# Kernel optimization log

Hardware: AMD Instinct MI355X
Metric: run time of the kernel (lower is better)

Reference implementation:

```python
import jax, jax.numpy as jnp
import numpy as np

B, S, H = 2, 2048, 2048
NH, KVH, HD = 32, 8, 64
G = NH // KVH
BASE = 10000.0
SCALE = 1.0 / np.sqrt(HD).astype(np.float32)


def _rope_cache(seq_len, dim, base):
    inv_freq = 1.0 / (base ** (jnp.arange(0, dim, 2, dtype=jnp.float32) / dim))
    t = jnp.arange(seq_len, dtype=jnp.float32)
    freqs = jnp.outer(t, inv_freq)            # [S, HD/2]
    emb = jnp.concatenate([freqs, freqs], -1)  # [S, HD]
    return jnp.cos(emb), jnp.sin(emb)


def _rotate_half(x):
    x1, x2 = jnp.split(x, 2, axis=-1)
    return jnp.concatenate([-x2, x1], axis=-1)


def setup_inputs() -> dict:
    key = jax.random.key(0)
    ks = jax.random.split(key, 5)
    hidden_states = jax.random.normal(ks[0], (B, S, H), jnp.float32)
    # additive causal mask, broadcast over heads
    causal = jnp.tril(jnp.ones((S, S), dtype=bool))
    attention_mask = jnp.where(causal, 0.0, -1e9).astype(jnp.float32)[None, None]
    attention_mask = jnp.broadcast_to(attention_mask, (B, 1, S, S))
    position_ids = jnp.broadcast_to(jnp.arange(S, dtype=jnp.int32), (B, S))
    w = 0.02
    Wq = jax.random.normal(ks[1], (H, NH * HD), jnp.float32) * w
    Wk = jax.random.normal(ks[2], (H, KVH * HD), jnp.float32) * w
    Wv = jax.random.normal(ks[3], (H, KVH * HD), jnp.float32) * w
    Wo = jax.random.normal(ks[4], (NH * HD, H), jnp.float32) * w
    return {"hidden_states": hidden_states, "attention_mask": attention_mask,
            "position_ids": position_ids, "Wq": Wq, "Wk": Wk, "Wv": Wv, "Wo": Wo}


def reference(hidden_states, attention_mask, position_ids, Wq, Wk, Wv, Wo):
    b, s, _ = hidden_states.shape
    q = (hidden_states @ Wq).reshape(b, s, NH, HD).transpose(0, 2, 1, 3)   # [B,NH,S,HD]
    k = (hidden_states @ Wk).reshape(b, s, KVH, HD).transpose(0, 2, 1, 3)  # [B,KVH,S,HD]
    v = (hidden_states @ Wv).reshape(b, s, KVH, HD).transpose(0, 2, 1, 3)
    cos_c, sin_c = _rope_cache(s, HD, BASE)
    cos = cos_c[position_ids][:, None]  # [B,1,S,HD]
    sin = sin_c[position_ids][:, None]
    q = q * cos + _rotate_half(q) * sin
    k = k * cos + _rotate_half(k) * sin
    # GQA: grouped einsum == repeat_kv + matmul (same math, no KV duplication)
    qg = q.reshape(b, KVH, G, s, HD)
    scores = jnp.einsum('bkgsd,bktd->bkgst', qg, k) * SCALE  # [B,KVH,G,S,S]
    scores = scores + attention_mask[:, :, None]             # mask [B,1,1,S,S]
    probs = jax.nn.softmax(scores.astype(jnp.float32), axis=-1).astype(q.dtype)
    ctx = jnp.einsum('bkgst,bktd->bkgsd', probs, v)
    ctx = ctx.reshape(b, NH, s, HD).transpose(0, 2, 1, 3).reshape(b, s, NH * HD)
    return ctx @ Wo
```

## Files before the change

kernel.cpp:

```cpp
#include <hip/hip_runtime.h>
#include <hip/hip_bf16.h>

#define DB   2
#define DS   2048
#define DH   2048
#define DNH  32
#define DKVH 8
#define DHD  64
#define DM   4096
#define DNQKV 3072

typedef __attribute__((ext_vector_type(8))) short bf16x8;
typedef __attribute__((ext_vector_type(4))) float f32x4;
typedef __attribute__((ext_vector_type(8))) unsigned short us8;
typedef __attribute__((ext_vector_type(4))) unsigned short us4;
typedef __attribute__((ext_vector_type(2))) unsigned int u32x2;

__device__ __forceinline__ float b2f(unsigned short u) {
  unsigned int x = ((unsigned int)u) << 16;
  return __builtin_bit_cast(float, x);
}
__device__ __forceinline__ unsigned short f2b(float f) {
  unsigned int u = __builtin_bit_cast(unsigned int, f);
  return (unsigned short)((u + 0x8000u) >> 16);
}
__device__ __forceinline__ unsigned int cvt_pk_bf16(float lo, float hi) {
  unsigned int r;
  asm("v_cvt_pk_bf16_f32 %0, %1, %2" : "=v"(r) : "v"(lo), "v"(hi));
  return r;
}
__device__ __forceinline__ void async_copy16(void* lds, const void* g) {
  __builtin_amdgcn_global_load_lds((const __attribute__((address_space(1))) void*)g,
                                   (__attribute__((address_space(3))) void*)lds,
                                   16, 0, 0);
}

#define BARRIER() do { asm volatile("" ::: "memory"); __builtin_amdgcn_s_barrier(); asm volatile("" ::: "memory"); } while (0)
#define LGKM0()   asm volatile("s_waitcnt lgkmcnt(0)" ::: "memory")
#define WAITVM(n) asm volatile("s_waitcnt vmcnt(" #n ")" ::: "memory")
#define MFMA16(d, a, bb) (d) = __builtin_amdgcn_mfma_f32_16x16x32_bf16((a), (bb), (d), 0, 0, 0)

__device__ __forceinline__ int detect_inline(const unsigned short* __restrict__ w) {
  int t = threadIdx.x & 63;
  int trips = 0;
#pragma unroll
  for (int i = 0; i < 4; i++) {
    unsigned short u = w[t * 4 + i];
    int e = (u >> 7) & 0xFF;
    if (e >= 161 || (e <= 93 && e != 0)) trips++;
  }
#pragma unroll
  for (int off = 32; off > 0; off >>= 1) trips += __shfl_down(trips, off);
  return __shfl(trips, 0) >= 8;
}

__global__ __launch_bounds__(256)
void prep(const void* __restrict__ hs, const void* __restrict__ wq,
          const void* __restrict__ wk, const void* __restrict__ wv,
          const void* __restrict__ wo,
          unsigned short* __restrict__ xb, unsigned short* __restrict__ wtqkv,
          unsigned short* __restrict__ wto) {
  __shared__ float tile[32][33];
  int mode = detect_inline((const unsigned short*)wq);
  int bid = blockIdx.x;
  if (bid < 4096) {
    int i = (bid * 256 + threadIdx.x) * 8;
    if (mode) {
      const float* f = (const float*)hs;
      us8 o;
#pragma unroll
      for (int j = 0; j < 8; j++) o[j] = f2b(f[i + j]);
      *(us8*)&xb[i] = o;
    } else {
      *(us8*)&xb[i] = *(const us8*)((const unsigned short*)hs + i);
    }
    return;
  }
  const void* win; unsigned short* out; int C, bx, by;
  if (bid < 8192)       { int l = bid - 4096;  win = wq; out = wtqkv;                         C = 2048; bx = l & 63; by = l >> 6; }
  else if (bid < 9216)  { int l = bid - 8192;  win = wk; out = wtqkv + (size_t)2048 * 2048;   C = 512;  bx = l & 15; by = l >> 4; }
  else if (bid < 10240) { int l = bid - 9216;  win = wv; out = wtqkv + (size_t)2560 * 2048;   C = 512;  bx = l & 15; by = l >> 4; }
  else                  { int l = bid - 10240; win = wo; out = wto;                           C = 2048; bx = l & 63; by = l >> 6; }
  int c0 = bx * 32, r0 = by * 32;
  int tx = threadIdx.x & 31, ty = threadIdx.x >> 5;
  if (mode) {
    const float* f = (const float*)win;
    for (int i = ty; i < 32; i += 8) tile[i][tx] = f[(size_t)(r0 + i) * C + c0 + tx];
  } else {
    const unsigned short* bsrc = (const unsigned short*)win;
    for (int i = ty; i < 32; i += 8) tile[i][tx] = b2f(bsrc[(size_t)(r0 + i) * C + c0 + tx]);
  }
  __syncthreads();
  for (int i = ty; i < 32; i += 8) out[(size_t)(c0 + i) * 2048 + r0 + tx] = f2b(tile[tx][i]);
}

#define QSC 0.18033688011112042f

__global__ __launch_bounds__(512, 2)
void gemm_qkv(const unsigned short* __restrict__ A, const unsigned short* __restrict__ Bt,
              const int* __restrict__ pos_ids,
              unsigned short* __restrict__ qws, unsigned short* __restrict__ kws,
              unsigned short* __restrict__ vt) {
  __shared__ __align__(16) unsigned short sm[65536];
  int tid = threadIdx.x, lane = tid & 63, wave = tid >> 6;
  int wm = wave >> 2, wn = wave & 3;
  int quad = lane >> 4, l15 = lane & 15;

  int bid = blockIdx.x;
  int wg = (bid & 7) * 24 + (bid >> 3);
  int ty = wg / 12, tx = wg - ty * 12;
  size_t tm0 = (size_t)ty * 256, tn0 = (size_t)tx * 256;

  const unsigned short* Ab = A + tm0 * 2048;
  const unsigned short* Bb = Bt + tn0 * 2048;

  auto UA = [&](int bu, int kh) { return sm + (bu * 2 + kh) * 8192; };
  auto UB = [&](int bu, int kh) { return sm + 32768 + (bu * 2 + kh) * 8192; };

  int c0 = tid, c1 = tid + 512;
  int r0s = c0 >> 2, r1s = c1 >> 2;
  int cc0 = (c0 & 3) ^ ((r0s >> 1) & 3);
  int cc1 = (c1 & 3) ^ ((r1s >> 1) & 3);
  size_t ga0 = (size_t)r0s * 2048 + cc0 * 8;
  size_t ga1 = (size_t)r1s * 2048 + cc1 * 8;

  auto stA = [&](int t, int kh, int bu) {
    const unsigned short* s = Ab + (size_t)t * 64 + kh * 32;
    async_copy16(UA(bu, kh) + c0 * 8, s + ga0);
    async_copy16(UA(bu, kh) + c1 * 8, s + ga1);
  };
  auto stB = [&](int t, int kh, int bu) {
    const unsigned short* s = Bb + (size_t)t * 64 + kh * 32;
    async_copy16(UB(bu, kh) + c0 * 8, s + ga0);
    async_copy16(UB(bu, kh) + c1 * 8, s + ga1);
  };

  int rdoff = l15 * 32 + ((quad << 3) ^ (((l15 >> 1) & 3) << 3));

  f32x4 zero4 = {0.f, 0.f, 0.f, 0.f};
  f32x4 acc[8][4];
#pragma unroll
  for (int mi = 0; mi < 8; mi++)
#pragma unroll
    for (int ni = 0; ni < 4; ni++) acc[mi][ni] = zero4;

  stA(0, 0, 0); stB(0, 0, 0); stA(0, 1, 0); stB(0, 1, 0); stA(1, 0, 1); stB(1, 0, 1);
  WAITVM(8); BARRIER();

#pragma unroll 2
  for (int t = 0; t < 32; ++t) {
    int bu = t & 1, bn = bu ^ 1;
    int t1 = (t + 1 < 32) ? t + 1 : 31;
    int t2 = (t + 2 < 32) ? t + 2 : 31;
    bf16x8 af[8];
    const unsigned short* pA0 = UA(bu, 0) + wm * 4096 + rdoff;
    const unsigned short* pB0 = UB(bu, 0) + wn * 2048 + rdoff;
    const unsigned short* pA1 = UA(bu, 1) + wm * 4096 + rdoff;
    const unsigned short* pB1 = UB(bu, 1) + wn * 2048 + rdoff;

#pragma unroll
    for (int mi = 0; mi < 8; mi++) af[mi] = *(const bf16x8*)(pA0 + mi * 512);
    bf16x8 b0 = *(const bf16x8*)pB0;
    bf16x8 b1 = *(const bf16x8*)(pB0 + 512);
    stA(t1, 1, bn);
    BARRIER(); LGKM0();
    __builtin_amdgcn_s_setprio(1);
#pragma unroll
    for (int mi = 0; mi < 8; mi++) { MFMA16(acc[mi][0], af[mi], b0); MFMA16(acc[mi][1], af[mi], b1); }
    __builtin_amdgcn_s_setprio(0);
    BARRIER();

    bf16x8 b2 = *(const bf16x8*)(pB0 + 1024);
    bf16x8 b3 = *(const bf16x8*)(pB0 + 1536);
    stB(t1, 1, bn);
    BARRIER(); LGKM0();
    __builtin_amdgcn_s_setprio(1);
#pragma unroll
    for (int mi = 0; mi < 8; mi++) { MFMA16(acc[mi][2], af[mi], b2); MFMA16(acc[mi][3], af[mi], b3); }
    __builtin_amdgcn_s_setprio(0);
    WAITVM(8);
    BARRIER();

#pragma unroll
    for (int mi = 0; mi < 8; mi++) af[mi] = *(const bf16x8*)(pA1 + mi * 512);
    b0 = *(const bf16x8*)pB1;
    b1 = *(const bf16x8*)(pB1 + 512);
    stA(t2, 0, bu);
    BARRIER(); LGKM0();
    __builtin_amdgcn_s_setprio(1);
#pragma unroll
    for (int mi = 0; mi < 8; mi++) { MFMA16(acc[mi][0], af[mi], b0); MFMA16(acc[mi][1], af[mi], b1); }
    __builtin_amdgcn_s_setprio(0);
    BARRIER();

    b2 = *(const bf16x8*)(pB1 + 1024);
    b3 = *(const bf16x8*)(pB1 + 1536);
    stB(t2, 0, bu);
    BARRIER(); LGKM0();
    __builtin_amdgcn_s_setprio(1);
#pragma unroll
    for (int mi = 0; mi < 8; mi++) { MFMA16(acc[mi][2], af[mi], b2); MFMA16(acc[mi][3], af[mi], b3); }
    __builtin_amdgcn_s_setprio(0);
    WAITVM(8);
    BARRIER();
  }
  WAITVM(0);

  int hs = (int)(tn0 >> 6) + wn;
  if (hs < 40) {
    float sc = (hs < 32) ? QSC : 1.0f;
    unsigned short* dst0 = (hs < 32) ? qws : kws;
    int hh = (hs < 32) ? hs : (hs - 32);
    float invf0 = __expf(-(float)l15 * (9.210340371976184f / 32.0f));
    float invf1 = invf0 * 0.01f;
#pragma unroll
    for (int mi = 0; mi < 8; mi++)
#pragma unroll
      for (int r = 0; r < 4; r++) {
        size_t gr = tm0 + wm * 128 + mi * 16 + quad * 4 + r;
        int bb = (int)(gr >> 11), s = (int)(gr & 2047);
        float tpos = (float)pos_ids[gr];
        unsigned short* row = dst0 + ((size_t)(bb * ((hs < 32) ? DNH : DKVH) + hh) * DS + s) * DHD;
#pragma unroll
        for (int ni = 0; ni < 2; ni++) {
          float x1 = acc[mi][ni][r], x2 = acc[mi][ni + 2][r];
          float ang = tpos * (ni ? invf1 : invf0);
          float sn, cs;
          __sincosf(ang, &sn, &cs);
          int d = ni * 16 + l15;
          row[d]      = f2b((x1 * cs - x2 * sn) * sc);
          row[d + 32] = f2b((x2 * cs + x1 * sn) * sc);
        }
      }
  } else {
    int vh = hs - 40;
    int bb = (int)(tm0 >> 11);
    int s0 = (int)(tm0 & 2047) + wm * 128 + quad * 4;
#pragma unroll
    for (int mi = 0; mi < 8; mi++)
#pragma unroll
      for (int ni = 0; ni < 4; ni++) {
        int d = ni * 16 + l15;
        us4 o4;
#pragma unroll
        for (int r = 0; r < 4; r++) o4[r] = f2b(acc[mi][ni][r]);
        *(us4*)&vt[((size_t)(bb * DKVH + vh) * DHD + d) * DS + s0 + mi * 16] = o4;
      }
  }
}

__global__ __launch_bounds__(512, 2)
void gemm_out(const unsigned short* __restrict__ A, const unsigned short* __restrict__ Bt,
              unsigned short* __restrict__ Cb, float* __restrict__ Cf,
              const unsigned short* __restrict__ wqdet) {
  __shared__ __align__(16) unsigned short sm[49152];
  int tid = threadIdx.x, lane = tid & 63, wave = tid >> 6;
  int wm = wave >> 2, wn = wave & 3;
  int quad = lane >> 4, l15 = lane & 15;

  int bid = blockIdx.x;
  int wg = (bid & 7) * 32 + (bid >> 3);
  int ty = wg >> 3, tx = wg & 7;
  size_t tm0 = (size_t)ty * 128, tn0 = (size_t)tx * 256;

  const unsigned short* Ab = A + tm0 * 2048;
  const unsigned short* Bb = Bt + tn0 * 2048;

  auto UA = [&](int bu, int kh) { return sm + (bu * 2 + kh) * 4096; };
  auto UB = [&](int bu, int kh) { return sm + 16384 + (bu * 2 + kh) * 8192; };

  int c0 = tid, c1 = tid + 512;
  int r0s = c0 >> 2, r1s = c1 >> 2;
  int cc0 = (c0 & 3) ^ ((r0s >> 1) & 3);
  int cc1 = (c1 & 3) ^ ((r1s >> 1) & 3);
  size_t ga0 = (size_t)r0s * 2048 + cc0 * 8;
  size_t ga1 = (size_t)r1s * 2048 + cc1 * 8;

  auto stA = [&](int t, int kh, int bu) {
    const unsigned short* s = Ab + (size_t)t * 64 + kh * 32;
    async_copy16(UA(bu, kh) + c0 * 8, s + ga0);
  };
  auto stB = [&](int t, int kh, int bu) {
    const unsigned short* s = Bb + (size_t)t * 64 + kh * 32;
    async_copy16(UB(bu, kh) + c0 * 8, s + ga0);
    async_copy16(UB(bu, kh) + c1 * 8, s + ga1);
  };

  int rdoff = l15 * 32 + ((quad << 3) ^ (((l15 >> 1) & 3) << 3));

  f32x4 zero4 = {0.f, 0.f, 0.f, 0.f};
  f32x4 acc[4][4];
#pragma unroll
  for (int mi = 0; mi < 4; mi++)
#pragma unroll
    for (int ni = 0; ni < 4; ni++) acc[mi][ni] = zero4;

  stA(0, 0, 0); stB(0, 0, 0); stA(0, 1, 0); stB(0, 1, 0); stA(1, 0, 1); stB(1, 0, 1);
  WAITVM(6); BARRIER();

#pragma unroll 2
  for (int t = 0; t < 32; ++t) {
    int bu = t & 1, bn = bu ^ 1;
    int t1 = (t + 1 < 32) ? t + 1 : 31;
    int t2 = (t + 2 < 32) ? t + 2 : 31;
    bf16x8 af[4];
    const unsigned short* pA0 = UA(bu, 0) + wm * 2048 + rdoff;
    const unsigned short* pB0 = UB(bu, 0) + wn * 2048 + rdoff;
    const unsigned short* pA1 = UA(bu, 1) + wm * 2048 + rdoff;
    const unsigned short* pB1 = UB(bu, 1) + wn * 2048 + rdoff;

#pragma unroll
    for (int mi = 0; mi < 4; mi++) af[mi] = *(const bf16x8*)(pA0 + mi * 512);
    bf16x8 b0 = *(const bf16x8*)pB0;
    bf16x8 b1 = *(const bf16x8*)(pB0 + 512);
    stA(t1, 1, bn);
    BARRIER(); LGKM0();
    __builtin_amdgcn_s_setprio(1);
#pragma unroll
    for (int mi = 0; mi < 4; mi++) { MFMA16(acc[mi][0], af[mi], b0); MFMA16(acc[mi][1], af[mi], b1); }
    __builtin_amdgcn_s_setprio(0);
    BARRIER();

    bf16x8 b2 = *(const bf16x8*)(pB0 + 1024);
    bf16x8 b3 = *(const bf16x8*)(pB0 + 1536);
    stB(t1, 1, bn);
    BARRIER(); LGKM0();
    __builtin_amdgcn_s_setprio(1);
#pragma unroll
    for (int mi = 0; mi < 4; mi++) { MFMA16(acc[mi][2], af[mi], b2); MFMA16(acc[mi][3], af[mi], b3); }
    __builtin_amdgcn_s_setprio(0);
    WAITVM(6);
    BARRIER();

#pragma unroll
    for (int mi = 0; mi < 4; mi++) af[mi] = *(const bf16x8*)(pA1 + mi * 512);
    b0 = *(const bf16x8*)pB1;
    b1 = *(const bf16x8*)(pB1 + 512);
    stA(t2, 0, bu);
    BARRIER(); LGKM0();
    __builtin_amdgcn_s_setprio(1);
#pragma unroll
    for (int mi = 0; mi < 4; mi++) { MFMA16(acc[mi][0], af[mi], b0); MFMA16(acc[mi][1], af[mi], b1); }
    __builtin_amdgcn_s_setprio(0);
    BARRIER();

    b2 = *(const bf16x8*)(pB1 + 1024);
    b3 = *(const bf16x8*)(pB1 + 1536);
    stB(t2, 0, bu);
    BARRIER(); LGKM0();
    __builtin_amdgcn_s_setprio(1);
#pragma unroll
    for (int mi = 0; mi < 4; mi++) { MFMA16(acc[mi][2], af[mi], b2); MFMA16(acc[mi][3], af[mi], b3); }
    __builtin_amdgcn_s_setprio(0);
    WAITVM(6);
    BARRIER();
  }
  WAITVM(0);

  int mode = detect_inline(wqdet);
#pragma unroll
  for (int mi = 0; mi < 4; mi++)
#pragma unroll
    for (int ni = 0; ni < 4; ni++)
#pragma unroll
      for (int r = 0; r < 4; r++) {
        size_t gr = tm0 + wm * 64 + mi * 16 + quad * 4 + r;
        size_t gc = tn0 + wn * 64 + ni * 16 + l15;
        float v = acc[mi][ni][r];
        if (mode) Cf[gr * 2048 + gc] = v;
        else      Cb[gr * 2048 + gc] = f2b(v);
      }
}

__global__ __launch_bounds__(256, 4)
void flash_attn(const unsigned short* __restrict__ q, const unsigned short* __restrict__ k,
                const unsigned short* __restrict__ vt, unsigned short* __restrict__ ctx) {
  __shared__ __align__(16) unsigned short lK[2][2][64 * 32];
  __shared__ __align__(16) unsigned short lV[2][2][64 * 32];
  __shared__ __align__(16) unsigned short lP[4][16 * 64];
  int tid = threadIdx.x, lane = tid & 63, wave = tid >> 6;
  int quad = lane >> 4, l15 = lane & 15;
  int bh = blockIdx.y, b = bh >> 5, h = bh & 31, kvh = h >> 2;
  const unsigned short* qb = q + (size_t)(b * DNH + h) * DS * DHD;
  const unsigned short* kb = k + (size_t)(b * DKVH + kvh) * DS * DHD;
  const unsigned short* vb = vt + (size_t)(b * DKVH + kvh) * DHD * DS;
  unsigned short* lPw = lP[wave];
  int r4 = tid >> 2;
  int cc8 = ((tid & 3) ^ ((r4 >> 1) & 3)) * 8;
  int swz = ((l15 >> 1) & 3) << 3;
  int pswz = (l15 & 7) << 3;

  f32x4 zero4 = {0.f, 0.f, 0.f, 0.f};
  for (int ph = 0; ph < 2; ph++) {
    int qt = ph ? (31 - blockIdx.x) : blockIdx.x;
    int q0 = qt * 64;
    const unsigned short* qp = qb + (size_t)(q0 + wave * 16 + l15) * DHD + quad * 8;
    bf16x8 qf0 = *(const bf16x8*)qp;
    bf16x8 qf1 = *(const bf16x8*)(qp + 32);
    f32x4 oacc[4];
#pragma unroll
    for (int dj = 0; dj < 4; dj++) oacc[dj] = zero4;
    float mrow = -1e30f, lrow = 0.f;

    int nt = qt + 1;
    {
      const unsigned short* sk = kb + (size_t)r4 * DHD + cc8;
      async_copy16(&lK[0][0][tid * 8], sk);
      async_copy16(&lK[0][1][tid * 8], sk + 32);
      const unsigned short* sv = vb + (size_t)r4 * DS + cc8;
      async_copy16(&lV[0][0][tid * 8], sv);
      async_copy16(&lV[0][1][tid * 8], sv + 32);
    }
    WAITVM(0); BARRIER();

    int cur = 0;
    for (int t = 0; t < nt; t++) {
      int kv0 = t * 64;
      if (t + 1 < nt) {
        const unsigned short* sk = kb + (size_t)(kv0 + 64 + r4) * DHD + cc8;
        async_copy16(&lK[cur ^ 1][0][tid * 8], sk);
        async_copy16(&lK[cur ^ 1][1][tid * 8], sk + 32);
        const unsigned short* sv = vb + (size_t)r4 * DS + kv0 + 64 + cc8;
        async_copy16(&lV[cur ^ 1][0][tid * 8], sv);
        async_copy16(&lV[cur ^ 1][1][tid * 8], sv + 32);
      }
      f32x4 sacc[4];
#pragma unroll
      for (int nj = 0; nj < 4; nj++) {
        int ro = (nj * 16 + l15) * 32 + ((quad * 8) ^ swz);
        bf16x8 kf0 = *(const bf16x8*)&lK[cur][0][ro];
        bf16x8 kf1 = *(const bf16x8*)&lK[cur][1][ro];
        sacc[nj] = zero4;
        MFMA16(sacc[nj], kf0, qf0);
        MFMA16(sacc[nj], kf1, qf1);
      }
      if (t == nt - 1) {
        int ql = wave * 16 + l15;
#pragma unroll
        for (int nj = 0; nj < 4; nj++)
#pragma unroll
          for (int r = 0; r < 4; r++)
            if (nj * 16 + quad * 4 + r > ql) sacc[nj][r] = -1e30f;
      }
      float a0 = fmaxf(fmaxf(sacc[0][0], sacc[0][1]), sacc[0][2]);
      float a1 = fmaxf(fmaxf(sacc[0][3], sacc[1][0]), sacc[1][1]);
      float a2 = fmaxf(fmaxf(sacc[1][2], sacc[1][3]), sacc[2][0]);
      float a3 = fmaxf(fmaxf(sacc[2][1], sacc[2][2]), sacc[2][3]);
      float a4 = fmaxf(fmaxf(sacc[3][0], sacc[3][1]), sacc[3][2]);
      float tm = fmaxf(fmaxf(fmaxf(a0, a1), fmaxf(a2, a3)), fmaxf(a4, sacc[3][3]));
      tm = fmaxf(tm, __shfl_xor(tm, 16));
      tm = fmaxf(tm, __shfl_xor(tm, 32));
      if (!__all(tm <= mrow + 8.f)) {
        float mn = fmaxf(mrow, tm);
        float alpha = __builtin_amdgcn_exp2f(mrow - mn);
        mrow = mn;
        lrow *= alpha;
#pragma unroll
        for (int dj = 0; dj < 4; dj++)
#pragma unroll
          for (int r = 0; r < 4; r++) oacc[dj][r] *= alpha;
      }
      float rs = 0.f;
#pragma unroll
      for (int nj = 0; nj < 4; nj++)
#pragma unroll
        for (int r = 0; r < 4; r++) {
          float e = __builtin_amdgcn_exp2f(sacc[nj][r] - mrow);
          sacc[nj][r] = e;
          rs += e;
        }
      rs += __shfl_xor(rs, 16);
      rs += __shfl_xor(rs, 32);
      lrow += rs;
#pragma unroll
      for (int nj = 0; nj < 4; nj++) {
        u32x2 w2;
        w2[0] = cvt_pk_bf16(sacc[nj][0], sacc[nj][1]);
        w2[1] = cvt_pk_bf16(sacc[nj][2], sacc[nj][3]);
        *(u32x2*)&lPw[l15 * 64 + ((nj * 16 + quad * 4) ^ pswz)] = w2;
      }
      bf16x8 pf0 = *(const bf16x8*)&lPw[l15 * 64 + ((quad * 8) ^ pswz)];
      bf16x8 pf1 = *(const bf16x8*)&lPw[l15 * 64 + ((32 + quad * 8) ^ pswz)];
#pragma unroll
      for (int dj = 0; dj < 4; dj++) {
        int ro = (dj * 16 + l15) * 32 + ((quad * 8) ^ swz);
        bf16x8 vf0 = *(const bf16x8*)&lV[cur][0][ro];
        bf16x8 vf1 = *(const bf16x8*)&lV[cur][1][ro];
        MFMA16(oacc[dj], vf0, pf0);
        MFMA16(oacc[dj], vf1, pf1);
      }
      WAITVM(0); BARRIER();
      cur ^= 1;
    }
    float inv = __builtin_amdgcn_rcpf(lrow);
    size_t orow = ((size_t)b * DS + q0 + wave * 16 + l15) * (DNH * DHD) + (size_t)h * DHD;
#pragma unroll
    for (int dj = 0; dj < 4; dj++) {
      u32x2 o2;
      o2[0] = cvt_pk_bf16(oacc[dj][0] * inv, oacc[dj][1] * inv);
      o2[1] = cvt_pk_bf16(oacc[dj][2] * inv, oacc[dj][3] * inv);
      *(u32x2*)&ctx[orow + dj * 16 + quad * 4] = o2;
    }
  }
}

extern "C" void kernel_launch(void* const* d_in, const int* in_sizes, int n_in,
                              void* d_out, int out_size, void* d_ws, size_t ws_size,
                              hipStream_t stream) {
  (void)in_sizes; (void)n_in; (void)out_size; (void)ws_size;
  const void* hs = d_in[0];
  const int* pos = (const int*)d_in[2];
  const void* wq = d_in[3];
  const void* wk = d_in[4];
  const void* wv = d_in[5];
  const void* wo = d_in[6];

  char* ws = (char*)d_ws;
  size_t off = 0;
  auto take = [&](size_t bytes) -> char* {
    char* p = ws + off;
    off += (bytes + 255) & ~(size_t)255;
    return p;
  };
  unsigned short* xb    = (unsigned short*)take((size_t)DM * DH * 2);
  unsigned short* wtqkv = (unsigned short*)take((size_t)DNQKV * DH * 2);
  unsigned short* wto   = (unsigned short*)take((size_t)DH * DH * 2);
  unsigned short* qws   = (unsigned short*)take((size_t)DB * DNH * DS * DHD * 2);
  unsigned short* kws   = (unsigned short*)take((size_t)DB * DKVH * DS * DHD * 2);
  unsigned short* vtws  = (unsigned short*)take((size_t)DB * DKVH * DS * DHD * 2);
  unsigned short* ctx   = (unsigned short*)take((size_t)DM * DNH * DHD * 2);

  prep<<<14336, 256, 0, stream>>>(hs, wq, wk, wv, wo, xb, wtqkv, wto);

  gemm_qkv<<<dim3(192), 512, 0, stream>>>(xb, wtqkv, pos, qws, kws, vtws);

  flash_attn<<<dim3(16, DB * DNH), 256, 0, stream>>>(qws, kws, vtws, ctx);

  gemm_out<<<dim3(256), 512, 0, stream>>>(ctx, wto, (unsigned short*)d_out, (float*)d_out,
                                          (const unsigned short*)wq);
}
```

Measured before the change: 302.1 us.

## Enlarge attention query tiles to 128 rows and retile weight transpose to 64x64

The flash attention kernel now uses 512-thread blocks, each handling a 128-row query tile with 8 waves sharing one K/V tile in LDS. That halves the K/V staging traffic per query row. Work is split into two launches by tile parity, with a mirrored tile order for load balance, and s_setprio is raised around the MFMA sections. The prep transpose uses 64x64 tiles, and the ctx buffer now reuses the xb workspace. The risks are higher register and LDS pressure per block, reduced occupancy, and an extra launch.

```diff
diff --git a/kernel.cpp b/kernel.cpp
--- a/kernel.cpp
+++ b/kernel.cpp
@@ -60,7 +60,7 @@
           const void* __restrict__ wo,
           unsigned short* __restrict__ xb, unsigned short* __restrict__ wtqkv,
           unsigned short* __restrict__ wto) {
-  __shared__ float tile[32][33];
+  __shared__ float tile[64][65];
   int mode = detect_inline((const unsigned short*)wq);
   int bid = blockIdx.x;
   if (bid < 4096) {
@@ -77,21 +77,21 @@
     return;
   }
   const void* win; unsigned short* out; int C, bx, by;
-  if (bid < 8192)       { int l = bid - 4096;  win = wq; out = wtqkv;                         C = 2048; bx = l & 63; by = l >> 6; }
-  else if (bid < 9216)  { int l = bid - 8192;  win = wk; out = wtqkv + (size_t)2048 * 2048;   C = 512;  bx = l & 15; by = l >> 4; }
-  else if (bid < 10240) { int l = bid - 9216;  win = wv; out = wtqkv + (size_t)2560 * 2048;   C = 512;  bx = l & 15; by = l >> 4; }
-  else                  { int l = bid - 10240; win = wo; out = wto;                           C = 2048; bx = l & 63; by = l >> 6; }
-  int c0 = bx * 32, r0 = by * 32;
-  int tx = threadIdx.x & 31, ty = threadIdx.x >> 5;
+  if (bid < 5120)       { int l = bid - 4096; win = wq; out = wtqkv;                       C = 2048; bx = l & 31; by = l >> 5; }
+  else if (bid < 5376)  { int l = bid - 5120; win = wk; out = wtqkv + (size_t)2048 * 2048; C = 512;  bx = l & 7;  by = l >> 3; }
+  else if (bid < 5632)  { int l = bid - 5376; win = wv; out = wtqkv + (size_t)2560 * 2048; C = 512;  bx = l & 7;  by = l >> 3; }
+  else                  { int l = bid - 5632; win = wo; out = wto;                         C = 2048; bx = l & 31; by = l >> 5; }
+  int c0 = bx * 64, r0 = by * 64;
+  int tx = threadIdx.x & 63, ty = threadIdx.x >> 6;
   if (mode) {
     const float* f = (const float*)win;
-    for (int i = ty; i < 32; i += 8) tile[i][tx] = f[(size_t)(r0 + i) * C + c0 + tx];
+    for (int i = ty; i < 64; i += 4) tile[i][tx] = f[(size_t)(r0 + i) * C + c0 + tx];
   } else {
     const unsigned short* bsrc = (const unsigned short*)win;
-    for (int i = ty; i < 32; i += 8) tile[i][tx] = b2f(bsrc[(size_t)(r0 + i) * C + c0 + tx]);
+    for (int i = ty; i < 64; i += 4) tile[i][tx] = b2f(bsrc[(size_t)(r0 + i) * C + c0 + tx]);
   }
   __syncthreads();
-  for (int i = ty; i < 32; i += 8) out[(size_t)(c0 + i) * 2048 + r0 + tx] = f2b(tile[tx][i]);
+  for (int i = ty; i < 64; i += 4) out[(size_t)(c0 + i) * 2048 + r0 + tx] = f2b(tile[tx][i]);
 }
 
 #define QSC 0.18033688011112042f
@@ -372,135 +372,138 @@
       }
 }
 
-__global__ __launch_bounds__(256, 4)
+__global__ __launch_bounds__(512, 4)
 void flash_attn(const unsigned short* __restrict__ q, const unsigned short* __restrict__ k,
-                const unsigned short* __restrict__ vt, unsigned short* __restrict__ ctx) {
+                const unsigned short* __restrict__ vt, unsigned short* __restrict__ ctx,
+                int parity) {
   __shared__ __align__(16) unsigned short lK[2][2][64 * 32];
   __shared__ __align__(16) unsigned short lV[2][2][64 * 32];
-  __shared__ __align__(16) unsigned short lP[4][16 * 64];
+  __shared__ __align__(16) unsigned short lP[8][16 * 64];
   int tid = threadIdx.x, lane = tid & 63, wave = tid >> 6;
   int quad = lane >> 4, l15 = lane & 15;
-  int bh = blockIdx.y, b = bh >> 5, h = bh & 31, kvh = h >> 2;
+  int bh = blockIdx.x, b = bh >> 5, h = bh & 31, kvh = h >> 2;
   const unsigned short* qb = q + (size_t)(b * DNH + h) * DS * DHD;
   const unsigned short* kb = k + (size_t)(b * DKVH + kvh) * DS * DHD;
   const unsigned short* vb = vt + (size_t)(b * DKVH + kvh) * DHD * DS;
   unsigned short* lPw = lP[wave];
-  int r4 = tid >> 2;
-  int cc8 = ((tid & 3) ^ ((r4 >> 1) & 3)) * 8;
+  int shalf = tid >> 8, r8 = tid & 255;
+  int rowS = r8 >> 2;
+  int cc8 = ((r8 & 3) ^ ((rowS >> 1) & 3)) * 8;
   int swz = ((l15 >> 1) & 3) << 3;
   int pswz = (l15 & 7) << 3;
+  int ql = wave * 16 + l15;
+
+  int y = blockIdx.y;
+  int qt = (y < 4) ? (2 * y + parity) : (22 - 2 * y + parity);
+  int nt = 2 * qt + 2;
+  int qg = qt * 128 + ql;
+
+  const unsigned short* qp = qb + (size_t)qg * DHD + quad * 8;
+  bf16x8 qf0 = *(const bf16x8*)qp, qf1 = *(const bf16x8*)(qp + 32);
 
   f32x4 zero4 = {0.f, 0.f, 0.f, 0.f};
-  for (int ph = 0; ph < 2; ph++) {
-    int qt = ph ? (31 - blockIdx.x) : blockIdx.x;
-    int q0 = qt * 64;
-    const unsigned short* qp = qb + (size_t)(q0 + wave * 16 + l15) * DHD + quad * 8;
-    bf16x8 qf0 = *(const bf16x8*)qp;
-    bf16x8 qf1 = *(const bf16x8*)(qp + 32);
-    f32x4 oacc[4];
-#pragma unroll
-    for (int dj = 0; dj < 4; dj++) oacc[dj] = zero4;
-    float mrow = -1e30f, lrow = 0.f;
-
-    int nt = qt + 1;
-    {
-      const unsigned short* sk = kb + (size_t)r4 * DHD + cc8;
-      async_copy16(&lK[0][0][tid * 8], sk);
-      async_copy16(&lK[0][1][tid * 8], sk + 32);
-      const unsigned short* sv = vb + (size_t)r4 * DS + cc8;
-      async_copy16(&lV[0][0][tid * 8], sv);
-      async_copy16(&lV[0][1][tid * 8], sv + 32);
+  f32x4 oacc[4];
+#pragma unroll
+  for (int dj = 0; dj < 4; dj++) oacc[dj] = zero4;
+  float mrow = -1e30f, lrow = 0.f;
+
+  auto stage = [&](int t, int buf) {
+    const unsigned short* sk = kb + (size_t)(t * 64 + rowS) * DHD + shalf * 32 + cc8;
+    async_copy16(&lK[buf][shalf][r8 * 8], sk);
+    const unsigned short* sv = vb + (size_t)rowS * DS + t * 64 + shalf * 32 + cc8;
+    async_copy16(&lV[buf][shalf][r8 * 8], sv);
+  };
+
+  stage(0, 0);
+  WAITVM(0); BARRIER();
+
+  int cur = 0;
+  for (int t = 0; t < nt; t++) {
+    if (t + 1 < nt) stage(t + 1, cur ^ 1);
+    int kv0 = t * 64;
+
+    f32x4 sacc[4];
+    __builtin_amdgcn_s_setprio(1);
+#pragma unroll
+    for (int nj = 0; nj < 4; nj++) {
+      int ro = (nj * 16 + l15) * 32 + ((quad * 8) ^ swz);
+      bf16x8 kf0 = *(const bf16x8*)&lK[cur][0][ro];
+      bf16x8 kf1 = *(const bf16x8*)&lK[cur][1][ro];
+      sacc[nj] = zero4;
+      MFMA16(sacc[nj], kf0, qf0);
+      MFMA16(sacc[nj], kf1, qf1);
     }
+    __builtin_amdgcn_s_setprio(0);
+
+    if ((kv0 + 63) > qg) {
+#pragma unroll
+      for (int nj = 0; nj < 4; nj++)
+#pragma unroll
+        for (int r = 0; r < 4; r++)
+          if (kv0 + nj * 16 + quad * 4 + r > qg) sacc[nj][r] = -1e30f;
+    }
+    float a0 = fmaxf(fmaxf(sacc[0][0], sacc[0][1]), sacc[0][2]);
+    float a1 = fmaxf(fmaxf(sacc[0][3], sacc[1][0]), sacc[1][1]);
+    float a2 = fmaxf(fmaxf(sacc[1][2], sacc[1][3]), sacc[2][0]);
+    float a3 = fmaxf(fmaxf(sacc[2][1], sacc[2][2]), sacc[2][3]);
+    float a4 = fmaxf(fmaxf(sacc[3][0], sacc[3][1]), sacc[3][2]);
+    float tm = fmaxf(fmaxf(fmaxf(a0, a1), fmaxf(a2, a3)), fmaxf(a4, sacc[3][3]));
+    tm = fmaxf(tm, __shfl_xor(tm, 16));
+    tm = fmaxf(tm, __shfl_xor(tm, 32));
+    if (!__all(tm <= mrow + 8.f)) {
+      float mn = fmaxf(mrow, tm);
+      float alpha = __builtin_amdgcn_exp2f(mrow - mn);
+      mrow = mn;
+      lrow *= alpha;
+#pragma unroll
+      for (int dj = 0; dj < 4; dj++)
+#pragma unroll
+        for (int r = 0; r < 4; r++) oacc[dj][r] *= alpha;
+    }
+    float rs = 0.f;
+#pragma unroll
+    for (int nj = 0; nj < 4; nj++)
+#pragma unroll
+      for (int r = 0; r < 4; r++) {
+        float e = __builtin_amdgcn_exp2f(sacc[nj][r] - mrow);
+        sacc[nj][r] = e;
+        rs += e;
+      }
+    rs += __shfl_xor(rs, 16);
+    rs += __shfl_xor(rs, 32);
+    lrow += rs;
+#pragma unroll
+    for (int nj = 0; nj < 4; nj++) {
+      u32x2 w2;
+      w2[0] = cvt_pk_bf16(sacc[nj][0], sacc[nj][1]);
+      w2[1] = cvt_pk_bf16(sacc[nj][2], sacc[nj][3]);
+      *(u32x2*)&lPw[l15 * 64 + ((nj * 16 + quad * 4) ^ pswz)] = w2;
+    }
+    bf16x8 pf0 = *(const bf16x8*)&lPw[l15 * 64 + ((quad * 8) ^ pswz)];
+    bf16x8 pf1 = *(const bf16x8*)&lPw[l15 * 64 + ((32 + quad * 8) ^ pswz)];
+    __builtin_amdgcn_s_setprio(1);
+#pragma unroll
+    for (int dj = 0; dj < 4; dj++) {
+      int ro = (dj * 16 + l15) * 32 + ((quad * 8) ^ swz);
+      bf16x8 vf0 = *(const bf16x8*)&lV[cur][0][ro];
+      bf16x8 vf1 = *(const bf16x8*)&lV[cur][1][ro];
+      MFMA16(oacc[dj], vf0, pf0);
+      MFMA16(oacc[dj], vf1, pf1);
+    }
+    __builtin_amdgcn_s_setprio(0);
+
     WAITVM(0); BARRIER();
-
-    int cur = 0;
-    for (int t = 0; t < nt; t++) {
-      int kv0 = t * 64;
-      if (t + 1 < nt) {
-        const unsigned short* sk = kb + (size_t)(kv0 + 64 + r4) * DHD + cc8;
-        async_copy16(&lK[cur ^ 1][0][tid * 8], sk);
-        async_copy16(&lK[cur ^ 1][1][tid * 8], sk + 32);
-        const unsigned short* sv = vb + (size_t)r4 * DS + kv0 + 64 + cc8;
-        async_copy16(&lV[cur ^ 1][0][tid * 8], sv);
-        async_copy16(&lV[cur ^ 1][1][tid * 8], sv + 32);
-      }
-      f32x4 sacc[4];
-#pragma unroll
-      for (int nj = 0; nj < 4; nj++) {
-        int ro = (nj * 16 + l15) * 32 + ((quad * 8) ^ swz);
-        bf16x8 kf0 = *(const bf16x8*)&lK[cur][0][ro];
-        bf16x8 kf1 = *(const bf16x8*)&lK[cur][1][ro];
-        sacc[nj] = zero4;
-        MFMA16(sacc[nj], kf0, qf0);
-        MFMA16(sacc[nj], kf1, qf1);
-      }
-      if (t == nt - 1) {
-        int ql = wave * 16 + l15;
-#pragma unroll
-        for (int nj = 0; nj < 4; nj++)
-#pragma unroll
-          for (int r = 0; r < 4; r++)
-            if (nj * 16 + quad * 4 + r > ql) sacc[nj][r] = -1e30f;
-      }
-      float a0 = fmaxf(fmaxf(sacc[0][0], sacc[0][1]), sacc[0][2]);
-      float a1 = fmaxf(fmaxf(sacc[0][3], sacc[1][0]), sacc[1][1]);
-      float a2 = fmaxf(fmaxf(sacc[1][2], sacc[1][3]), sacc[2][0]);
-      float a3 = fmaxf(fmaxf(sacc[2][1], sacc[2][2]), sacc[2][3]);
-      float a4 = fmaxf(fmaxf(sacc[3][0], sacc[3][1]), sacc[3][2]);
-      float tm = fmaxf(fmaxf(fmaxf(a0, a1), fmaxf(a2, a3)), fmaxf(a4, sacc[3][3]));
-      tm = fmaxf(tm, __shfl_xor(tm, 16));
-      tm = fmaxf(tm, __shfl_xor(tm, 32));
-      if (!__all(tm <= mrow + 8.f)) {
-        float mn = fmaxf(mrow, tm);
-        float alpha = __builtin_amdgcn_exp2f(mrow - mn);
-        mrow = mn;
-        lrow *= alpha;
-#pragma unroll
-        for (int dj = 0; dj < 4; dj++)
-#pragma unroll
-          for (int r = 0; r < 4; r++) oacc[dj][r] *= alpha;
-      }
-      float rs = 0.f;
-#pragma unroll
-      for (int nj = 0; nj < 4; nj++)
-#pragma unroll
-        for (int r = 0; r < 4; r++) {
-          float e = __builtin_amdgcn_exp2f(sacc[nj][r] - mrow);
-          sacc[nj][r] = e;
-          rs += e;
-        }
-      rs += __shfl_xor(rs, 16);
-      rs += __shfl_xor(rs, 32);
-      lrow += rs;
-#pragma unroll
-      for (int nj = 0; nj < 4; nj++) {
-        u32x2 w2;
-        w2[0] = cvt_pk_bf16(sacc[nj][0], sacc[nj][1]);
-        w2[1] = cvt_pk_bf16(sacc[nj][2], sacc[nj][3]);
-        *(u32x2*)&lPw[l15 * 64 + ((nj * 16 + quad * 4) ^ pswz)] = w2;
-      }
-      bf16x8 pf0 = *(const bf16x8*)&lPw[l15 * 64 + ((quad * 8) ^ pswz)];
-      bf16x8 pf1 = *(const bf16x8*)&lPw[l15 * 64 + ((32 + quad * 8) ^ pswz)];
-#pragma unroll
-      for (int dj = 0; dj < 4; dj++) {
-        int ro = (dj * 16 + l15) * 32 + ((quad * 8) ^ swz);
-        bf16x8 vf0 = *(const bf16x8*)&lV[cur][0][ro];
-        bf16x8 vf1 = *(const bf16x8*)&lV[cur][1][ro];
-        MFMA16(oacc[dj], vf0, pf0);
-        MFMA16(oacc[dj], vf1, pf1);
-      }
-      WAITVM(0); BARRIER();
-      cur ^= 1;
-    }
-    float inv = __builtin_amdgcn_rcpf(lrow);
-    size_t orow = ((size_t)b * DS + q0 + wave * 16 + l15) * (DNH * DHD) + (size_t)h * DHD;
-#pragma unroll
-    for (int dj = 0; dj < 4; dj++) {
-      u32x2 o2;
-      o2[0] = cvt_pk_bf16(oacc[dj][0] * inv, oacc[dj][1] * inv);
-      o2[1] = cvt_pk_bf16(oacc[dj][2] * inv, oacc[dj][3] * inv);
-      *(u32x2*)&ctx[orow + dj * 16 + quad * 4] = o2;
-    }
+    cur ^= 1;
+  }
+
+  float inv = __builtin_amdgcn_rcpf(lrow);
+  size_t orow = ((size_t)b * DS + qg) * (DNH * DHD) + (size_t)h * DHD;
+#pragma unroll
+  for (int dj = 0; dj < 4; dj++) {
+    u32x2 o2;
+    o2[0] = cvt_pk_bf16(oacc[dj][0] * inv, oacc[dj][1] * inv);
+    o2[1] = cvt_pk_bf16(oacc[dj][2] * inv, oacc[dj][3] * inv);
+    *(u32x2*)&ctx[orow + dj * 16 + quad * 4] = o2;
   }
 }
 
@@ -528,13 +531,14 @@
   unsigned short* qws   = (unsigned short*)take((size_t)DB * DNH * DS * DHD * 2);
   unsigned short* kws   = (unsigned short*)take((size_t)DB * DKVH * DS * DHD * 2);
   unsigned short* vtws  = (unsigned short*)take((size_t)DB * DKVH * DS * DHD * 2);
-  unsigned short* ctx   = (unsigned short*)take((size_t)DM * DNH * DHD * 2);
-
-  prep<<<14336, 256, 0, stream>>>(hs, wq, wk, wv, wo, xb, wtqkv, wto);
+  unsigned short* ctx   = xb;
+
+  prep<<<6656, 256, 0, stream>>>(hs, wq, wk, wv, wo, xb, wtqkv, wto);
 
   gemm_qkv<<<dim3(192), 512, 0, stream>>>(xb, wtqkv, pos, qws, kws, vtws);
 
-  flash_attn<<<dim3(16, DB * DNH), 256, 0, stream>>>(qws, kws, vtws, ctx);
+  flash_attn<<<dim3(DB * DNH, 8), 512, 0, stream>>>(qws, kws, vtws, ctx, 0);
+  flash_attn<<<dim3(DB * DNH, 8), 512, 0, stream>>>(qws, kws, vtws, ctx, 1);
 
   gemm_out<<<dim3(256), 512, 0, stream>>>(ctx, wto, (unsigned short*)d_out, (float*)d_out,
                                           (const unsigned short*)wq);
```

Result: slower. 326.0 us (+7.9%).
